# Performance work log

Measured on AMD Instinct MI355X. Metric: run time of the kernel, lower is better.

## Reference

```python
import jax, jax.numpy as jnp
import numpy as np

E, K = 8, 2          # n_experts, top-k
D, O = 768, 3072     # input_size, output_size
B, S = 4, 512        # batch, seq


def setup_inputs() -> dict:
    key = jax.random.key(0)
    k1, k2, k3, k4, k5 = jax.random.split(key, 5)
    x = jax.random.normal(k1, (B, S, D), jnp.float32)
    w_gate = jax.random.normal(k2, (D, E), jnp.float32) * 0.02
    expert_w = jax.random.normal(k3, (E, O, D), jnp.float32) * 0.02
    expert_b = jax.random.normal(k4, (E, O), jnp.float32) * 0.02
    static_w = jax.random.normal(k5, (O, D), jnp.float32) * 0.02
    return {"x": x, "w_gate": w_gate, "expert_w": expert_w,
            "expert_b": expert_b, "static_w": static_w}


def cv_squared(v):
    # torch .var() is unbiased (ddof=1)
    return jnp.var(v, ddof=1) / (jnp.mean(v) ** 2 + 1e-10)


def reference(x, w_gate, expert_w, expert_b, static_w):
    loss_coef = 0.01
    xf = x.reshape(-1, D)                      # [N, D]
    N = xf.shape[0]

    # --- top-k gating (eval path: no noise) ---
    logits = xf @ w_gate                       # [N, E]
    top_v, top_i = jax.lax.top_k(logits, K + 1)
    top_k_gates = jax.nn.softmax(top_v[:, :K], axis=1)   # [N, K]
    gates = jnp.zeros_like(logits).at[
        jnp.arange(N)[:, None], top_i[:, :K]].set(top_k_gates)  # [N, E]

    importance = gates.sum(0)                  # [E]
    load = (gates > 0).sum(0).astype(jnp.float32)
    loss = (cv_squared(importance) + cv_squared(load)) * loss_coef

    # --- experts: F.linear(h, W_e + static_w, b_e), combined by gates ---
    W = expert_w + static_w[None]              # [E, O, D]
    y_e = jnp.einsum('nd,eod->neo', xf, W) + expert_b[None]   # [N, E, O]
    y = jnp.einsum('neo,ne->no', y_e, gates)   # [N, O]

    return y.reshape(B, S, O), loss
```

## Files before the change

### kernel.cpp

```cpp
#include <hip/hip_runtime.h>
#include <hip/hip_bf16.h>
#include <stdint.h>

#define E_ 8
#define D_ 768
#define O_ 3072
#define N_ 2048

typedef __attribute__((ext_vector_type(8))) __bf16 bf16x8;
typedef __attribute__((ext_vector_type(4))) float f32x4;

__device__ __forceinline__ unsigned short f2bf(float f) {
    union { float f; uint32_t u; } a; a.f = f;
    uint32_t u = a.u;
    uint32_t r = (u + 0x7fffu + ((u >> 16) & 1u)) >> 16;
    return (unsigned short)r;
}

__device__ __forceinline__ void async16(const void* g, void* l) {
    __builtin_amdgcn_global_load_lds(
        (const __attribute__((address_space(1))) void*)g,
        (__attribute__((address_space(3))) void*)l, 16, 0, 0);
}

__global__ __launch_bounds__(256) void prologue_kernel(
    const float* __restrict__ x, const float* __restrict__ w_gate,
    const float* __restrict__ ew, const float* __restrict__ sw,
    unsigned short* __restrict__ xb, unsigned short* __restrict__ wb,
    int* __restrict__ choice_e, float* __restrict__ choice_g,
    float* __restrict__ y)
{
    if (blockIdx.x >= 512) {
        int i = (blockIdx.x - 512) * 256 + threadIdx.x;
        int f = i * 8;
        const int od = O_ * D_;
        int e = f / od;
        int rem = f - e * od;
        float4 a0 = *(const float4*)(ew + f);
        float4 a1 = *(const float4*)(ew + f + 4);
        float4 b0 = *(const float4*)(sw + rem);
        float4 b1 = *(const float4*)(sw + rem + 4);
        union { ushort u[8]; uint4 v; } o;
        o.u[0] = f2bf(a0.x + b0.x); o.u[1] = f2bf(a0.y + b0.y);
        o.u[2] = f2bf(a0.z + b0.z); o.u[3] = f2bf(a0.w + b0.w);
        o.u[4] = f2bf(a1.x + b1.x); o.u[5] = f2bf(a1.y + b1.y);
        o.u[6] = f2bf(a1.z + b1.z); o.u[7] = f2bf(a1.w + b1.w);
        ((uint4*)wb)[i] = o.v;
        return;
    }

    int wid  = threadIdx.x >> 6;
    int lane = threadIdx.x & 63;
    int n = blockIdx.x * 4 + wid;
    const float* xr = x + (size_t)n * D_;

    float acc[E_];
#pragma unroll
    for (int e = 0; e < E_; ++e) acc[e] = 0.f;

    for (int c = 0; c < D_ / 64; ++c) {
        int d = c * 64 + lane;
        float xv = xr[d];
        xb[(size_t)n * D_ + d] = f2bf(xv);
        const float* wg = w_gate + (size_t)d * E_;
        float4 w0 = *(const float4*)(wg);
        float4 w1 = *(const float4*)(wg + 4);
        acc[0] += xv * w0.x; acc[1] += xv * w0.y;
        acc[2] += xv * w0.z; acc[3] += xv * w0.w;
        acc[4] += xv * w1.x; acc[5] += xv * w1.y;
        acc[6] += xv * w1.z; acc[7] += xv * w1.w;
    }
#pragma unroll
    for (int e = 0; e < E_; ++e) {
        float v = acc[e];
        for (int off = 32; off > 0; off >>= 1) v += __shfl_xor(v, off, 64);
        acc[e] = v;
    }
    if (lane == 0) {
        int i0 = 0; float v0 = acc[0];
#pragma unroll
        for (int e = 1; e < E_; ++e) if (acc[e] > v0) { v0 = acc[e]; i0 = e; }
        int i1 = -1; float v1 = -3.0e38f;
#pragma unroll
        for (int e = 0; e < E_; ++e) if (e != i0 && acc[e] > v1) { v1 = acc[e]; i1 = e; }
        float ex = expf(v1 - v0);
        float g0 = 1.f / (1.f + ex);
        float g1 = ex / (1.f + ex);
        choice_e[2 * n]     = i0;  choice_g[2 * n]     = g0;
        choice_e[2 * n + 1] = i1;  choice_g[2 * n + 1] = g1;
    }

    float4 z = {0.f, 0.f, 0.f, 0.f};
    float4* yb = (float4*)(y + (size_t)blockIdx.x * 12288);
#pragma unroll
    for (int i = 0; i < 12; ++i) yb[threadIdx.x + 256 * i] = z;
}

__global__ __launch_bounds__(1024) void compact_kernel(
    const int* __restrict__ choice_e, const float* __restrict__ choice_g,
    int* __restrict__ counts, int* __restrict__ pair_token,
    float* __restrict__ pair_gate, float* __restrict__ out_loss)
{
    __shared__ int   s_cnt[E_];
    __shared__ float s_imp[E_];
    int t = threadIdx.x;
    int lane = t & 63;
    if (t < E_) s_cnt[t] = 0;
    __syncthreads();

#pragma unroll
    for (int it = 0; it < (2 * N_) / 1024; ++it) {
        int i = it * 1024 + t;
        int ce = choice_e[i];
        float gv = choice_g[i];
        unsigned long long mask[E_];
#pragma unroll
        for (int e = 0; e < E_; ++e) mask[e] = __ballot(ce == e);
        int b = 0;
        if (lane < E_) b = atomicAdd(&s_cnt[lane], __popcll(mask[lane]));
        int mybase = __shfl(b, ce, 64);
        unsigned long long mymask = mask[0];
#pragma unroll
        for (int e = 1; e < E_; ++e) if (ce == e) mymask = mask[e];
        int pos = mybase + __popcll(mymask & ((1ull << lane) - 1ull));
        pair_token[ce * N_ + pos] = i >> 1;
        pair_gate[ce * N_ + pos]  = gv;
    }
    __syncthreads();
    if (t < E_) counts[t] = s_cnt[t];

    if (t < 256) {
        int e = t >> 5, l = t & 31;
        int cnt = s_cnt[e];
        float p = 0.f;
        for (int i = l; i < cnt; i += 32) p += pair_gate[e * N_ + i];
#pragma unroll
        for (int off = 16; off > 0; off >>= 1) p += __shfl_down(p, off, 32);
        if (l == 0) s_imp[e] = p;
    }
    __syncthreads();
    if (t == 0) {
        float mi = 0.f, ml = 0.f, imp[E_], ld[E_];
#pragma unroll
        for (int i = 0; i < E_; ++i) {
            imp[i] = s_imp[i]; ld[i] = (float)s_cnt[i];
            mi += imp[i]; ml += ld[i];
        }
        mi /= (float)E_; ml /= (float)E_;
        float vi = 0.f, vl = 0.f;
#pragma unroll
        for (int i = 0; i < E_; ++i) {
            vi += (imp[i] - mi) * (imp[i] - mi);
            vl += (ld[i] - ml) * (ld[i] - ml);
        }
        vi /= (float)(E_ - 1); vl /= (float)(E_ - 1);
        *out_loss = 0.01f * (vi / (mi * mi + 1e-10f) + vl / (ml * ml + 1e-10f));
    }
}

#define BM 128
#define BN 128
#define BK 64

__global__ __launch_bounds__(256) void moe_gemm_kernel(
    const unsigned short* __restrict__ xb,
    const unsigned short* __restrict__ wb,
    const float* __restrict__ expert_b,
    const int* __restrict__ counts,
    const int* __restrict__ pair_token,
    const float* __restrict__ pair_gate,
    float* __restrict__ y)
{
    int e = blockIdx.z;
    int cnt = counts[e];
    int m0 = blockIdx.y * BM;
    if (m0 >= cnt) return;
    int n0 = blockIdx.x * BN;

    __shared__ __align__(16) unsigned short sA[2][BM * BK];
    __shared__ __align__(16) unsigned short sB[2][BN * BK];

    int tid  = threadIdx.x;
    int lane = tid & 63;
    int wid  = tid >> 6;
    int wm = wid & 1, wn = wid >> 1;
    int l16 = lane & 15;
    int quad = lane >> 4;

    int r0 = tid >> 3;
    int kg = (tid & 7) ^ (r0 & 7);
    const unsigned short* gA[4];
    const unsigned short* gB[4];
#pragma unroll
    for (int s = 0; s < 4; ++s) {
        int row = r0 + 32 * s;
        int ar = m0 + row; if (ar >= cnt) ar = cnt - 1;
        gA[s] = xb + (size_t)pair_token[e * N_ + ar] * D_ + kg * 8;
        gB[s] = wb + ((size_t)e * O_ + n0 + row) * D_ + kg * 8;
    }
    char* lA[2] = { (char*)sA[0] + wid * 1024, (char*)sA[1] + wid * 1024 };
    char* lB[2] = { (char*)sB[0] + wid * 1024, (char*)sB[1] + wid * 1024 };

    f32x4 acc[4][4];
#pragma unroll
    for (int a = 0; a < 4; ++a)
#pragma unroll
        for (int b = 0; b < 4; ++b) acc[a][b] = (f32x4){0.f, 0.f, 0.f, 0.f};

#pragma unroll
    for (int s = 0; s < 4; ++s) {
        async16(gA[s], lA[0] + s * 4096);
        async16(gB[s], lB[0] + s * 4096);
    }

    int kb = 0;
    for (int k0 = 0; k0 < D_; k0 += BK, kb ^= 1) {
        __syncthreads();
        int kn = k0 + BK;
        if (kn < D_) {
#pragma unroll
            for (int s = 0; s < 4; ++s) {
                async16(gA[s] + kn, lA[kb ^ 1] + s * 4096);
                async16(gB[s] + kn, lB[kb ^ 1] + s * 4096);
            }
        }
#pragma unroll
        for (int ks = 0; ks < 2; ++ks) {
            bf16x8 af[4], bfr[4];
#pragma unroll
            for (int mi = 0; mi < 4; ++mi) {
                int row = wm * 64 + mi * 16 + l16;
                int ch  = row * 8 + ((ks * 4 + quad) ^ (row & 7));
                af[mi] = *(const bf16x8*)&sA[kb][ch * 8];
            }
#pragma unroll
            for (int ni = 0; ni < 4; ++ni) {
                int row = wn * 64 + ni * 16 + l16;
                int ch  = row * 8 + ((ks * 4 + quad) ^ (row & 7));
                bfr[ni] = *(const bf16x8*)&sB[kb][ch * 8];
            }
#pragma unroll
            for (int mi = 0; mi < 4; ++mi)
#pragma unroll
                for (int ni = 0; ni < 4; ++ni)
                    acc[mi][ni] = __builtin_amdgcn_mfma_f32_16x16x32_bf16(
                        af[mi], bfr[ni], acc[mi][ni], 0, 0, 0);
        }
    }

    float bias[4];
#pragma unroll
    for (int ni = 0; ni < 4; ++ni)
        bias[ni] = expert_b[e * O_ + n0 + wn * 64 + ni * 16 + l16];
#pragma unroll
    for (int mi = 0; mi < 4; ++mi) {
        int rb = m0 + wm * 64 + mi * 16 + quad * 4;
#pragma unroll
        for (int reg = 0; reg < 4; ++reg) {
            int r = rb + reg;
            if (r < cnt) {
                int token  = pair_token[e * N_ + r];
                float gate = pair_gate[e * N_ + r];
#pragma unroll
                for (int ni = 0; ni < 4; ++ni) {
                    int o = n0 + wn * 64 + ni * 16 + l16;
                    atomicAdd(&y[(size_t)token * O_ + o],
                              gate * (acc[mi][ni][reg] + bias[ni]));
                }
            }
        }
    }
}

extern "C" void kernel_launch(void* const* d_in, const int* in_sizes, int n_in,
                              void* d_out, int out_size, void* d_ws, size_t ws_size,
                              hipStream_t stream) {
    const float* x        = (const float*)d_in[0];
    const float* w_gate   = (const float*)d_in[1];
    const float* expert_w = (const float*)d_in[2];
    const float* expert_b = (const float*)d_in[3];
    const float* static_w = (const float*)d_in[4];
    float* out = (float*)d_out;

    char* ws = (char*)d_ws;
    int*   counts     = (int*)(ws + 0);
    int*   pair_token = (int*)(ws + 4096);
    float* pair_gate  = (float*)(ws + 4096 + 65536);
    int*   choice_e   = (int*)(ws + 4096 + 131072);
    float* choice_g   = (float*)(ws + 4096 + 131072 + 16384);
    unsigned short* xb = (unsigned short*)(ws + 4096 + 131072 + 32768);
    unsigned short* wb = (unsigned short*)(ws + 4096 + 131072 + 32768 + 3145728);

    prologue_kernel<<<512 + (E_ * O_ * D_ / 8) / 256, 256, 0, stream>>>(
        x, w_gate, expert_w, static_w, xb, wb, choice_e, choice_g, out);
    compact_kernel<<<1, 1024, 0, stream>>>(choice_e, choice_g, counts,
                                           pair_token, pair_gate, out + (size_t)N_ * O_);

    dim3 grid(O_ / BN, N_ / BM, E_);
    moe_gemm_kernel<<<grid, 256, 0, stream>>>(xb, wb, expert_b, counts,
                                              pair_token, pair_gate, out);
}
```

Measured before the change: 215.2 us.

## Replace atomic scatter with per-slot bf16 partials and a separate reduce kernel

The GEMM epilogue now writes each token-expert slot's gated result as bf16 into a per-pair partial buffer instead of doing fp32 atomicAdd into the output. A new reduce kernel sums the two partials per token into the output, so zeroing the output in the prologue is no longer needed. This is meant to remove atomic contention and scattered read-modify-write traffic. In exchange it adds a kernel launch and an extra pass over a 2N×O bf16 buffer, and rounding the partials to bf16 costs precision.

```diff
diff --git a/kernel.cpp b/kernel.cpp
--- a/kernel.cpp
+++ b/kernel.cpp
@@ -16,6 +16,12 @@
     uint32_t r = (u + 0x7fffu + ((u >> 16) & 1u)) >> 16;
     return (unsigned short)r;
 }
+__device__ __forceinline__ float bflo(uint32_t u) {
+    union { uint32_t u; float f; } a; a.u = u << 16; return a.f;
+}
+__device__ __forceinline__ float bfhi(uint32_t u) {
+    union { uint32_t u; float f; } a; a.u = u & 0xffff0000u; return a.f;
+}
 
 __device__ __forceinline__ void async16(const void* g, void* l) {
     __builtin_amdgcn_global_load_lds(
@@ -27,8 +33,7 @@
     const float* __restrict__ x, const float* __restrict__ w_gate,
     const float* __restrict__ ew, const float* __restrict__ sw,
     unsigned short* __restrict__ xb, unsigned short* __restrict__ wb,
-    int* __restrict__ choice_e, float* __restrict__ choice_g,
-    float* __restrict__ y)
+    int* __restrict__ choice_e, float* __restrict__ choice_g)
 {
     if (blockIdx.x >= 512) {
         int i = (blockIdx.x - 512) * 256 + threadIdx.x;
@@ -89,16 +94,11 @@
         choice_e[2 * n]     = i0;  choice_g[2 * n]     = g0;
         choice_e[2 * n + 1] = i1;  choice_g[2 * n + 1] = g1;
     }
-
-    float4 z = {0.f, 0.f, 0.f, 0.f};
-    float4* yb = (float4*)(y + (size_t)blockIdx.x * 12288);
-#pragma unroll
-    for (int i = 0; i < 12; ++i) yb[threadIdx.x + 256 * i] = z;
 }
 
 __global__ __launch_bounds__(1024) void compact_kernel(
     const int* __restrict__ choice_e, const float* __restrict__ choice_g,
-    int* __restrict__ counts, int* __restrict__ pair_token,
+    int* __restrict__ counts, int* __restrict__ pair_id,
     float* __restrict__ pair_gate, float* __restrict__ out_loss)
 {
     __shared__ int   s_cnt[E_];
@@ -123,8 +123,8 @@
 #pragma unroll
         for (int e = 1; e < E_; ++e) if (ce == e) mymask = mask[e];
         int pos = mybase + __popcll(mymask & ((1ull << lane) - 1ull));
-        pair_token[ce * N_ + pos] = i >> 1;
-        pair_gate[ce * N_ + pos]  = gv;
+        pair_id[ce * N_ + pos]   = i;
+        pair_gate[ce * N_ + pos] = gv;
     }
     __syncthreads();
     if (t < E_) counts[t] = s_cnt[t];
@@ -167,9 +167,9 @@
     const unsigned short* __restrict__ wb,
     const float* __restrict__ expert_b,
     const int* __restrict__ counts,
-    const int* __restrict__ pair_token,
+    const int* __restrict__ pair_id,
     const float* __restrict__ pair_gate,
-    float* __restrict__ y)
+    unsigned short* __restrict__ part)
 {
     int e = blockIdx.z;
     int cnt = counts[e];
@@ -195,7 +195,7 @@
     for (int s = 0; s < 4; ++s) {
         int row = r0 + 32 * s;
         int ar = m0 + row; if (ar >= cnt) ar = cnt - 1;
-        gA[s] = xb + (size_t)pair_token[e * N_ + ar] * D_ + kg * 8;
+        gA[s] = xb + (size_t)(pair_id[e * N_ + ar] >> 1) * D_ + kg * 8;
         gB[s] = wb + ((size_t)e * O_ + n0 + row) * D_ + kg * 8;
     }
     char* lA[2] = { (char*)sA[0] + wid * 1024, (char*)sA[1] + wid * 1024 };
@@ -259,17 +259,35 @@
         for (int reg = 0; reg < 4; ++reg) {
             int r = rb + reg;
             if (r < cnt) {
-                int token  = pair_token[e * N_ + r];
+                int pid    = pair_id[e * N_ + r];
                 float gate = pair_gate[e * N_ + r];
 #pragma unroll
                 for (int ni = 0; ni < 4; ++ni) {
                     int o = n0 + wn * 64 + ni * 16 + l16;
-                    atomicAdd(&y[(size_t)token * O_ + o],
-                              gate * (acc[mi][ni][reg] + bias[ni]));
+                    part[(size_t)pid * O_ + o] =
+                        f2bf(gate * (acc[mi][ni][reg] + bias[ni]));
                 }
             }
         }
     }
+}
+
+__global__ __launch_bounds__(256) void reduce_kernel(
+    const unsigned short* __restrict__ part, float* __restrict__ y)
+{
+    int i = blockIdx.x * 256 + threadIdx.x;
+    int n = i / (O_ / 8);
+    int c = (i - n * (O_ / 8)) * 8;
+    const uint4 p0 = *(const uint4*)(part + (size_t)(2 * n) * O_ + c);
+    const uint4 p1 = *(const uint4*)(part + (size_t)(2 * n + 1) * O_ + c);
+    float4 o0, o1;
+    o0.x = bflo(p0.x) + bflo(p1.x); o0.y = bfhi(p0.x) + bfhi(p1.x);
+    o0.z = bflo(p0.y) + bflo(p1.y); o0.w = bfhi(p0.y) + bfhi(p1.y);
+    o1.x = bflo(p0.z) + bflo(p1.z); o1.y = bfhi(p0.z) + bfhi(p1.z);
+    o1.z = bflo(p0.w) + bflo(p1.w); o1.w = bfhi(p0.w) + bfhi(p1.w);
+    float* yp = y + (size_t)n * O_ + c;
+    *(float4*)(yp)     = o0;
+    *(float4*)(yp + 4) = o1;
 }
 
 extern "C" void kernel_launch(void* const* d_in, const int* in_sizes, int n_in,
@@ -283,20 +301,23 @@
     float* out = (float*)d_out;
 
     char* ws = (char*)d_ws;
-    int*   counts     = (int*)(ws + 0);
-    int*   pair_token = (int*)(ws + 4096);
-    float* pair_gate  = (float*)(ws + 4096 + 65536);
-    int*   choice_e   = (int*)(ws + 4096 + 131072);
-    float* choice_g   = (float*)(ws + 4096 + 131072 + 16384);
-    unsigned short* xb = (unsigned short*)(ws + 4096 + 131072 + 32768);
-    unsigned short* wb = (unsigned short*)(ws + 4096 + 131072 + 32768 + 3145728);
+    int*   counts    = (int*)(ws + 0);
+    int*   pair_id   = (int*)(ws + 4096);
+    float* pair_gate = (float*)(ws + 69632);
+    int*   choice_e  = (int*)(ws + 135168);
+    float* choice_g  = (float*)(ws + 151552);
+    unsigned short* xb   = (unsigned short*)(ws + 167936);
+    unsigned short* wb   = (unsigned short*)(ws + 3313664);
+    unsigned short* part = (unsigned short*)(ws + 41062400);
 
     prologue_kernel<<<512 + (E_ * O_ * D_ / 8) / 256, 256, 0, stream>>>(
-        x, w_gate, expert_w, static_w, xb, wb, choice_e, choice_g, out);
+        x, w_gate, expert_w, static_w, xb, wb, choice_e, choice_g);
     compact_kernel<<<1, 1024, 0, stream>>>(choice_e, choice_g, counts,
-                                           pair_token, pair_gate, out + (size_t)N_ * O_);
+                                           pair_id, pair_gate, out + (size_t)N_ * O_);
 
     dim3 grid(O_ / BN, N_ / BM, E_);
     moe_gemm_kernel<<<grid, 256, 0, stream>>>(xb, wb, expert_b, counts,
-                                              pair_token, pair_gate, out);
-}
+                                              pair_id, pair_gate, part);
+
+    reduce_kernel<<<(N_ * O_ / 8) / 256, 256, 0, stream>>>(part, out);
+}
```

Result: faster. 191.3 us (-11.1%).
